# Optimization experiments

Hardware: AMD Instinct MI355X
Metric: run time of the kernel (lower is better)

The kernel has to match this reference:

```python
import jax, jax.numpy as jnp
import numpy as np

WH, WW = 8, 8
N = WH * WW
DIM = 128
NUM_HEADS = 4
HEAD_DIM = DIM // NUM_HEADS
SCALE = HEAD_DIM ** -0.5


def _relative_position_index():
    coords = np.stack(np.meshgrid(np.arange(WH), np.arange(WW), indexing='ij'))  # (2, Wh, Ww)
    flat = coords.reshape(2, -1)  # (2, N)
    rel = flat[:, :, None] - flat[:, None, :]  # (2, N, N)
    rel = rel.transpose(1, 2, 0)  # (N, N, 2)
    rel[:, :, 0] += WH - 1
    rel[:, :, 1] += WW - 1
    rel[:, :, 0] *= 2 * WW - 1
    return rel.sum(-1)  # (N, N) int

REL_IDX = _relative_position_index()


def setup_inputs() -> dict:
    key = jax.random.key(0)
    ks = jax.random.split(key, 7)
    B_ = 4096
    nW = 64
    table_size = (2 * WH - 1) * (2 * WW - 1)  # 225
    return {
        'x': jax.random.normal(ks[0], (B_, N, DIM), dtype=jnp.float32),
        'mask': jax.random.normal(ks[1], (nW, N, N), dtype=jnp.float32),
        'qkv_w': jax.random.normal(ks[2], (3 * DIM, DIM), dtype=jnp.float32) * 0.02,
        'qkv_b': jnp.zeros((3 * DIM,), dtype=jnp.float32),
        'proj_w': jax.random.normal(ks[3], (DIM, DIM), dtype=jnp.float32) * 0.02,
        'proj_b': jnp.zeros((DIM,), dtype=jnp.float32),
        'bias_table': jax.random.normal(ks[4], (table_size, NUM_HEADS), dtype=jnp.float32) * 0.02,
    }


def reference(x, mask, qkv_w, qkv_b, proj_w, proj_b, bias_table):
    B_, n, C = x.shape
    nW = mask.shape[0]
    qkv = x @ qkv_w.T + qkv_b  # (B_, N, 3C)
    qkv = qkv.reshape(B_, n, 3, NUM_HEADS, HEAD_DIM)
    q = qkv[:, :, 0] * SCALE  # (B_, N, H, hd)
    k = qkv[:, :, 1]
    v = qkv[:, :, 2]
    attn = jnp.einsum('bihd,bjhd->bhij', q, k)  # (B_, H, N, N)
    rel_bias = bias_table[REL_IDX.reshape(-1)].reshape(n, n, NUM_HEADS)
    attn = attn + rel_bias.transpose(2, 0, 1)[None]  # broadcast over B_
    attn = attn.reshape(B_ // nW, nW, NUM_HEADS, n, n) + mask[None, :, None]
    attn = attn.reshape(B_, NUM_HEADS, n, n)
    attn = jax.nn.softmax(attn, axis=-1)
    out = jnp.einsum('bhij,bjhd->bihd', attn, v).reshape(B_, n, C)
    return out @ proj_w.T + proj_b
```

## Files before the change

### kernel.cpp

```cpp
#include <hip/hip_runtime.h>


typedef __bf16 bf16x8 __attribute__((ext_vector_type(8)));
typedef float f32x16 __attribute__((ext_vector_type(16)));

#define MFMA32(a, b, c) __builtin_amdgcn_mfma_f32_32x32x16_bf16(a, b, c, 0, 0, 0)
#define ATT_SCALE 0.17677669529663687f

__device__ __forceinline__ unsigned short f2bf(float f) {
  union { float fv; unsigned int u; } cv; cv.fv = f;
  unsigned int r = cv.u + 0x7FFFu + ((cv.u >> 16) & 1u);
  return (unsigned short)(r >> 16);
}

__device__ __forceinline__ unsigned pk2(float lo, float hi) {
  union { __bf16 h[2]; unsigned u; } t;
  t.h[0] = (__bf16)lo; t.h[1] = (__bf16)hi;
  return t.u;
}

__device__ __forceinline__ void pairw(float l0, float l1, float h0, float h1,
                                      int hl, unsigned &wlo, unsigned &whi) {
  unsigned lo = pk2(l0, l1);
  unsigned hi = pk2(h0, h1);
  unsigned los = (unsigned)__shfl_xor((int)lo, 32);
  unsigned his = (unsigned)__shfl_xor((int)hi, 32);
  wlo = hl ? his : lo;
  whi = hl ? hi : los;
}

__device__ __forceinline__ bf16x8 frag8(float a0, float a1, float a2, float a3,
                                        float a4, float a5, float a6, float a7,
                                        int hl) {
  union { unsigned u[4]; bf16x8 v; } r;
  pairw(a0, a1, a4, a5, hl, r.u[0], r.u[2]);
  pairw(a2, a3, a6, a7, hl, r.u[1], r.u[3]);
  return r.v;
}

#define FRAG_LO(p) frag8(p[0], p[1], p[2], p[3], p[4], p[5], p[6], p[7], hl)
#define FRAG_HI(p) frag8(p[8], p[9], p[10], p[11], p[12], p[13], p[14], p[15], hl)

__global__ __launch_bounds__(256) void convert_weights(
    const float* __restrict__ qkv_w, const float* __restrict__ proj_w,
    unsigned short* __restrict__ wq, unsigned short* __restrict__ wp) {
  int t = blockIdx.x * 256 + threadIdx.x;
  if (t < 384 * 128) {
    float v = qkv_w[t];
    if (t < 128 * 128) v *= ATT_SCALE;
    wq[t] = f2bf(v);
  } else {
    wp[t - 384 * 128] = f2bf(proj_w[t - 384 * 128]);
  }
}

__global__ __launch_bounds__(256) void build_cb(
    const float* __restrict__ mask, const float* __restrict__ bias_table,
    float* __restrict__ cb) {
  int t = blockIdx.x * 256 + threadIdx.x;
  int ij = t & 4095;
  int h = (t >> 12) & 3;
  int w = t >> 14;
  int j = ij >> 6, i = ij & 63;
  int ridx = ((i >> 3) - (j >> 3) + 7) * 15 + ((i & 7) - (j & 7) + 7);
  cb[t] = bias_table[ridx * 4 + h] + mask[(w << 12) + (i << 6) + j];
}

__global__ __launch_bounds__(256, 3) void window_attn(
    const float* __restrict__ x, const float* __restrict__ qkv_b,
    const float* __restrict__ proj_b, const unsigned short* __restrict__ wq,
    const unsigned short* __restrict__ wp, const float* __restrict__ cbT,
    float* __restrict__ out, int nW) {
  __shared__ unsigned short Xb[64][136];
  __shared__ unsigned short Vt[4][32][72];

  const int tid = threadIdx.x;
  const int h = tid >> 6;
  const int lane = tid & 63;
  const int l31 = lane & 31;
  const int hl = lane >> 5;
  const int b = blockIdx.x;
  const int w = b % nW;

  const float* xb = x + (size_t)b * 8192;
  #pragma unroll
  for (int st = 0; st < 8; ++st) {
    int e = (st * 256 + tid) * 4;
    float4 v4 = *reinterpret_cast<const float4*>(xb + e);
    ushort4 o;
    o.x = f2bf(v4.x); o.y = f2bf(v4.y); o.z = f2bf(v4.z); o.w = f2bf(v4.w);
    *reinterpret_cast<ushort4*>(&Xb[e >> 7][e & 127]) = o;
  }
  __syncthreads();

  {
    f32x16 av0, av1;
    #pragma unroll
    for (int q = 0; q < 16; ++q) { av0[q] = 0.0f; av1[q] = 0.0f; }
    const unsigned short* wvp = wq + (size_t)(256 + h * 32 + l31) * 128 + hl * 8;
    #pragma unroll
    for (int kt = 0; kt < 8; ++kt) {
      bf16x8 aw = *reinterpret_cast<const bf16x8*>(wvp + kt * 16);
      bf16x8 b0 = *reinterpret_cast<const bf16x8*>(&Xb[l31][kt * 16 + hl * 8]);
      bf16x8 b1 = *reinterpret_cast<const bf16x8*>(&Xb[32 + l31][kt * 16 + hl * 8]);
      av0 = MFMA32(aw, b0, av0);
      av1 = MFMA32(aw, b1, av1);
    }
    #pragma unroll
    for (int r = 0; r < 16; ++r) {
      int dr = (r & 3) + 8 * (r >> 2) + 4 * hl;
      float bv = qkv_b[256 + h * 32 + dr];
      Vt[h][dr][l31]      = f2bf(av0[r] + bv);
      Vt[h][dr][32 + l31] = f2bf(av1[r] + bv);
    }
  }

  bf16x8 qf[2][2], kf[2][2];
  {
    f32x16 aq[2], ak[2];
    #pragma unroll
    for (int t2 = 0; t2 < 2; ++t2)
      #pragma unroll
      for (int q = 0; q < 16; ++q) { aq[t2][q] = 0.0f; ak[t2][q] = 0.0f; }
    const unsigned short* wqp = wq + (size_t)(h * 32 + l31) * 128 + hl * 8;
    const unsigned short* wkp = wq + (size_t)(128 + h * 32 + l31) * 128 + hl * 8;
    #pragma unroll
    for (int kt = 0; kt < 8; ++kt) {
      bf16x8 b0 = *reinterpret_cast<const bf16x8*>(&Xb[l31][kt * 16 + hl * 8]);
      bf16x8 b1 = *reinterpret_cast<const bf16x8*>(&Xb[32 + l31][kt * 16 + hl * 8]);
      bf16x8 awq = *reinterpret_cast<const bf16x8*>(wqp + kt * 16);
      bf16x8 awk = *reinterpret_cast<const bf16x8*>(wkp + kt * 16);
      aq[0] = MFMA32(awq, b0, aq[0]);
      aq[1] = MFMA32(awq, b1, aq[1]);
      ak[0] = MFMA32(awk, b0, ak[0]);
      ak[1] = MFMA32(awk, b1, ak[1]);
    }
    __syncthreads();

    #pragma unroll
    for (int r = 0; r < 16; ++r) {
      int dr = (r & 3) + 8 * (r >> 2) + 4 * hl;
      float bq = qkv_b[h * 32 + dr] * ATT_SCALE;
      float bk = qkv_b[128 + h * 32 + dr];
      aq[0][r] += bq; aq[1][r] += bq;
      ak[0][r] += bk; ak[1][r] += bk;
    }

    #pragma unroll
    for (int t2 = 0; t2 < 2; ++t2) {
      kf[t2][0] = FRAG_LO(ak[t2]); kf[t2][1] = FRAG_HI(ak[t2]);
    }
    #pragma unroll
    for (int t2 = 0; t2 < 2; ++t2) {
      qf[t2][0] = FRAG_LO(aq[t2]); qf[t2][1] = FRAG_HI(aq[t2]);
    }
  }

  const float* cbp = cbT + (((size_t)w * 4 + h) << 12);
  #pragma unroll
  for (int it = 0; it < 2; ++it) {
    f32x16 s[2];
    #pragma unroll
    for (int mt = 0; mt < 2; ++mt)
      #pragma unroll
      for (int r = 0; r < 16; ++r) {
        int jr = (r & 3) + 8 * (r >> 2) + 4 * hl + 32 * mt;
        s[mt][r] = cbp[jr * 64 + 32 * it + l31];
      }
    #pragma unroll
    for (int mt = 0; mt < 2; ++mt) {
      s[mt] = MFMA32(kf[mt][0], qf[it][0], s[mt]);
      s[mt] = MFMA32(kf[mt][1], qf[it][1], s[mt]);
    }

    float mx[8];
    #pragma unroll
    for (int r = 0; r < 8; ++r)
      mx[r] = fmaxf(fmaxf(s[0][r], s[0][r + 8]), fmaxf(s[1][r], s[1][r + 8]));
    mx[0] = fmaxf(mx[0], mx[4]); mx[1] = fmaxf(mx[1], mx[5]);
    mx[2] = fmaxf(mx[2], mx[6]); mx[3] = fmaxf(mx[3], mx[7]);
    float m = fmaxf(fmaxf(mx[0], mx[1]), fmaxf(mx[2], mx[3]));
    m = fmaxf(m, __shfl_xor(m, 32));
    #pragma unroll
    for (int mt = 0; mt < 2; ++mt)
      #pragma unroll
      for (int r = 0; r < 16; ++r)
        s[mt][r] = __expf(s[mt][r] - m);
    float sm[8];
    #pragma unroll
    for (int r = 0; r < 8; ++r)
      sm[r] = (s[0][r] + s[0][r + 8]) + (s[1][r] + s[1][r + 8]);
    sm[0] += sm[4]; sm[1] += sm[5]; sm[2] += sm[6]; sm[3] += sm[7];
    float sum = (sm[0] + sm[1]) + (sm[2] + sm[3]);
    sum += __shfl_xor(sum, 32);
    const float rinv = __builtin_amdgcn_rcpf(sum);

    bf16x8 pf[4];
    pf[0] = FRAG_LO(s[0]); pf[1] = FRAG_HI(s[0]);
    pf[2] = FRAG_LO(s[1]); pf[3] = FRAG_HI(s[1]);

    f32x16 o;
    #pragma unroll
    for (int q = 0; q < 16; ++q) o[q] = 0.0f;
    #pragma unroll
    for (int kt = 0; kt < 4; ++kt) {
      bf16x8 aV = *reinterpret_cast<const bf16x8*>(&Vt[h][l31][kt * 16 + hl * 8]);
      o = MFMA32(aV, pf[kt], o);
    }
    #pragma unroll
    for (int r = 0; r < 16; ++r) {
      int dr = (r & 3) + 8 * (r >> 2) + 4 * hl;
      Xb[32 * it + l31][h * 32 + dr] = f2bf(o[r] * rinv);
    }
  }
  __syncthreads();

  {
    const int c = h * 32 + l31;
    const float pb = proj_b[c];
    const unsigned short* wrow = wp + (size_t)c * 128 + hl * 8;
    bf16x8 bfr[8];
    #pragma unroll
    for (int kt = 0; kt < 8; ++kt)
      bfr[kt] = *reinterpret_cast<const bf16x8*>(wrow + kt * 16);
    float* ob = out + (size_t)b * 8192;
    #pragma unroll
    for (int mt = 0; mt < 2; ++mt) {
      f32x16 acc;
      #pragma unroll
      for (int q = 0; q < 16; ++q) acc[q] = 0.0f;
      #pragma unroll
      for (int kt = 0; kt < 8; ++kt) {
        bf16x8 a = *reinterpret_cast<const bf16x8*>(&Xb[mt * 32 + l31][kt * 16 + hl * 8]);
        acc = MFMA32(a, bfr[kt], acc);
      }
      #pragma unroll
      for (int r = 0; r < 16; ++r) {
        int row = (r & 3) + 8 * (r >> 2) + 4 * hl + mt * 32;
        ob[row * 128 + c] = acc[r] + pb;
      }
    }
  }
}

extern "C" void kernel_launch(void* const* d_in, const int* in_sizes, int n_in,
                              void* d_out, int out_size, void* d_ws, size_t ws_size,
                              hipStream_t stream) {
  const float* x          = (const float*)d_in[0];
  const float* mask       = (const float*)d_in[1];
  const float* qkv_w      = (const float*)d_in[2];
  const float* qkv_b      = (const float*)d_in[3];
  const float* proj_w     = (const float*)d_in[4];
  const float* proj_b     = (const float*)d_in[5];
  const float* bias_table = (const float*)d_in[6];
  const int B_ = in_sizes[0] / 8192;
  const int nW = in_sizes[1] / 4096;

  unsigned short* wq = (unsigned short*)d_ws;
  unsigned short* wp = wq + 384 * 128;
  float* cbuf = (float*)((char*)d_ws + 131072);

  convert_weights<<<(384 * 128 + 128 * 128) / 256, 256, 0, stream>>>(qkv_w, proj_w, wq, wp);
  build_cb<<<(nW * 4 * 4096) / 256, 256, 0, stream>>>(mask, bias_table, cbuf);
  window_attn<<<B_, 256, 0, stream>>>(x, qkv_b, proj_b, wq, wp, cbuf, (float*)d_out, nW);
}
```

Baseline: 318.9 us.

## Merge prep kernels, split mask and rel-bias tables, and drop a barrier

The two setup kernels become one prep launch that transposes the mask per window, builds a per-head relative-bias table, and converts the weights with vectorized loads. The main kernel now reads mask and bias separately and adds them, which shrinks the precomputed table from nW*4*4096 to (nW+4)*4096 floats so it stays cache-resident, at the cost of a second load and an add. The attention output goes to a separate shared buffer Ob, which lets the barrier after the QK projection be removed, at the cost of extra LDS that may lower occupancy.

```diff
diff --git a/kernel.cpp b/kernel.cpp
--- a/kernel.cpp
+++ b/kernel.cpp
@@ -41,38 +41,66 @@
 #define FRAG_LO(p) frag8(p[0], p[1], p[2], p[3], p[4], p[5], p[6], p[7], hl)
 #define FRAG_HI(p) frag8(p[8], p[9], p[10], p[11], p[12], p[13], p[14], p[15], hl)
 
-__global__ __launch_bounds__(256) void convert_weights(
+__global__ __launch_bounds__(256) void prep(
+    const float* __restrict__ mask, const float* __restrict__ bias_table,
     const float* __restrict__ qkv_w, const float* __restrict__ proj_w,
+    float* __restrict__ maskT, float* __restrict__ relT,
     unsigned short* __restrict__ wq, unsigned short* __restrict__ wp) {
-  int t = blockIdx.x * 256 + threadIdx.x;
-  if (t < 384 * 128) {
-    float v = qkv_w[t];
-    if (t < 128 * 128) v *= ATT_SCALE;
-    wq[t] = f2bf(v);
+  const int blk = blockIdx.x;
+  const int tid = threadIdx.x;
+  if (blk < 64) {
+    __shared__ float T[64][65];
+    const float* mp = mask + (size_t)blk * 4096;
+    #pragma unroll
+    for (int rr = 0; rr < 16; ++rr) {
+      int e = rr * 256 + tid;
+      T[e >> 6][e & 63] = mp[e];
+    }
+    __syncthreads();
+    float* op = maskT + (size_t)blk * 4096;
+    #pragma unroll
+    for (int rr = 0; rr < 16; ++rr) {
+      int e = rr * 256 + tid;
+      op[e] = T[e & 63][e >> 6];
+    }
+  } else if (blk < 80) {
+    int t0 = (blk - 64) * 256 + tid;
+    #pragma unroll
+    for (int u = 0; u < 4; ++u) {
+      int t = u * 4096 + t0;
+      int ji = t & 4095;
+      int h = t >> 12;
+      int j = ji >> 6, i = ji & 63;
+      int ridx = ((i >> 3) - (j >> 3) + 7) * 15 + ((i & 7) - (j & 7) + 7);
+      relT[t] = bias_table[ridx * 4 + h];
+    }
   } else {
-    wp[t - 384 * 128] = f2bf(proj_w[t - 384 * 128]);
-  }
-}
-
-__global__ __launch_bounds__(256) void build_cb(
-    const float* __restrict__ mask, const float* __restrict__ bias_table,
-    float* __restrict__ cb) {
-  int t = blockIdx.x * 256 + threadIdx.x;
-  int ij = t & 4095;
-  int h = (t >> 12) & 3;
-  int w = t >> 14;
-  int j = ij >> 6, i = ij & 63;
-  int ridx = ((i >> 3) - (j >> 3) + 7) * 15 + ((i & 7) - (j & 7) + 7);
-  cb[t] = bias_table[ridx * 4 + h] + mask[(w << 12) + (i << 6) + j];
+    int t = ((blk - 80) * 256 + tid) * 4;
+    if (t < 49152) {
+      float4 v = *reinterpret_cast<const float4*>(qkv_w + t);
+      float sc = (t < 16384) ? ATT_SCALE : 1.0f;
+      ushort4 o;
+      o.x = f2bf(v.x * sc); o.y = f2bf(v.y * sc);
+      o.z = f2bf(v.z * sc); o.w = f2bf(v.w * sc);
+      *reinterpret_cast<ushort4*>(wq + t) = o;
+    } else {
+      int tp = t - 49152;
+      float4 v = *reinterpret_cast<const float4*>(proj_w + tp);
+      ushort4 o;
+      o.x = f2bf(v.x); o.y = f2bf(v.y); o.z = f2bf(v.z); o.w = f2bf(v.w);
+      *reinterpret_cast<ushort4*>(wp + tp) = o;
+    }
+  }
 }
 
 __global__ __launch_bounds__(256, 3) void window_attn(
     const float* __restrict__ x, const float* __restrict__ qkv_b,
     const float* __restrict__ proj_b, const unsigned short* __restrict__ wq,
-    const unsigned short* __restrict__ wp, const float* __restrict__ cbT,
-    float* __restrict__ out, int nW) {
+    const unsigned short* __restrict__ wp, const float* __restrict__ maskT,
+    const float* __restrict__ relT, float* __restrict__ out, int nW) {
   __shared__ unsigned short Xb[64][136];
   __shared__ unsigned short Vt[4][32][72];
+  __shared__ unsigned short Ob[64][136];
 
   const int tid = threadIdx.x;
   const int h = tid >> 6;
@@ -135,7 +163,6 @@
       ak[0] = MFMA32(awk, b0, ak[0]);
       ak[1] = MFMA32(awk, b1, ak[1]);
     }
-    __syncthreads();
 
     #pragma unroll
     for (int r = 0; r < 16; ++r) {
@@ -156,7 +183,8 @@
     }
   }
 
-  const float* cbp = cbT + (((size_t)w * 4 + h) << 12);
+  const float* mkp = maskT + ((size_t)w << 12);
+  const float* rlp = relT + ((size_t)h << 12);
   #pragma unroll
   for (int it = 0; it < 2; ++it) {
     f32x16 s[2];
@@ -164,8 +192,8 @@
     for (int mt = 0; mt < 2; ++mt)
       #pragma unroll
       for (int r = 0; r < 16; ++r) {
-        int jr = (r & 3) + 8 * (r >> 2) + 4 * hl + 32 * mt;
-        s[mt][r] = cbp[jr * 64 + 32 * it + l31];
+        int off = ((r & 3) + 8 * (r >> 2) + 4 * hl + 32 * mt) * 64 + 32 * it + l31;
+        s[mt][r] = mkp[off] + rlp[off];
       }
     #pragma unroll
     for (int mt = 0; mt < 2; ++mt) {
@@ -210,7 +238,7 @@
     #pragma unroll
     for (int r = 0; r < 16; ++r) {
       int dr = (r & 3) + 8 * (r >> 2) + 4 * hl;
-      Xb[32 * it + l31][h * 32 + dr] = f2bf(o[r] * rinv);
+      Ob[32 * it + l31][h * 32 + dr] = f2bf(o[r] * rinv);
     }
   }
   __syncthreads();
@@ -231,7 +259,7 @@
       for (int q = 0; q < 16; ++q) acc[q] = 0.0f;
       #pragma unroll
       for (int kt = 0; kt < 8; ++kt) {
-        bf16x8 a = *reinterpret_cast<const bf16x8*>(&Xb[mt * 32 + l31][kt * 16 + hl * 8]);
+        bf16x8 a = *reinterpret_cast<const bf16x8*>(&Ob[mt * 32 + l31][kt * 16 + hl * 8]);
         acc = MFMA32(a, bfr[kt], acc);
       }
       #pragma unroll
@@ -258,9 +286,9 @@
 
   unsigned short* wq = (unsigned short*)d_ws;
   unsigned short* wp = wq + 384 * 128;
-  float* cbuf = (float*)((char*)d_ws + 131072);
-
-  convert_weights<<<(384 * 128 + 128 * 128) / 256, 256, 0, stream>>>(qkv_w, proj_w, wq, wp);
-  build_cb<<<(nW * 4 * 4096) / 256, 256, 0, stream>>>(mask, bias_table, cbuf);
-  window_attn<<<B_, 256, 0, stream>>>(x, qkv_b, proj_b, wq, wp, cbuf, (float*)d_out, nW);
-}
+  float* maskT = (float*)((char*)d_ws + 131072);
+  float* relT  = (float*)((char*)d_ws + 131072 + (size_t)nW * 4096 * 4);
+
+  prep<<<144, 256, 0, stream>>>(mask, bias_table, qkv_w, proj_w, maskT, relT, wq, wp);
+  window_attn<<<B_, 256, 0, stream>>>(x, qkv_b, proj_b, wq, wp, maskT, relT, (float*)d_out, nW);
+}
```

Result: faster. 302.5 us (-5.1%).
